# Kernel tuning notes

Measured on AMD Instinct MI355X. Metric: run time of the kernel, lower is better.

## Reference

```python
import jax, jax.numpy as jnp
import numpy as np

T_SCALE = 160
NUM_SAMPLE = 32
FEAT_DIM = 2048
HIDDEN = 512
N_CLASS = 20
BATCH = 8


def build_sample_mask(tscale=T_SCALE, ns=NUM_SAMPLE):
    # Vectorized version of _get_interp1d_mask (prop_boundary_ratio=0, num_sample_perbin=1).
    # Returns mask of shape [tscale, ns, start, end] (already transposed as in the torch code).
    s = np.arange(tscale)[:, None, None]           # start
    e = np.arange(tscale)[None, :, None]           # end
    k = np.arange(ns)[None, None, :]
    pos = s + (e - s) * k / (ns - 1.0)             # [T, T, ns] sample positions
    Sg, Eg, Kg = np.broadcast_arrays(s, e, k)
    posf = pos.ravel(); Sf = Sg.ravel(); Ef = Eg.ravel(); Kf = Kg.ravel()
    valid = Ef >= Sf
    frac, dn = np.modf(posf)
    dn = dn.astype(np.int64)
    up = np.ceil(posf).astype(np.int64)
    mask = np.zeros((tscale, ns, tscale, tscale), dtype=np.float32)
    m1 = valid & (dn >= 0) & (dn <= tscale - 1)
    np.add.at(mask, (dn[m1], Kf[m1], Sf[m1], Ef[m1]), (1.0 - frac[m1]).astype(np.float32))
    m2 = valid & (up >= 0) & (up <= tscale - 1)
    np.add.at(mask, (up[m2], Kf[m2], Sf[m2], Ef[m2]), frac[m2].astype(np.float32))
    return jnp.asarray(mask)


def conv1d(x, w, padding):
    # x: [B, Cin, T], w: [Cout, Cin, K]
    return jax.lax.conv_general_dilated(
        x, w, window_strides=(1,), padding=[(padding, padding)],
        dimension_numbers=("NCH", "OIH", "NCH"))


def setup_inputs() -> dict:
    key = jax.random.key(0)
    ks = jax.random.split(key, 6)
    x = jax.random.normal(ks[0], (BATCH, T_SCALE, FEAT_DIM), dtype=jnp.float32)
    w1 = jax.random.normal(ks[1], (HIDDEN, FEAT_DIM, 3), dtype=jnp.float32) * 0.02
    b1 = jnp.zeros((HIDDEN,), dtype=jnp.float32)
    wc = jax.random.normal(ks[2], (N_CLASS, HIDDEN, 1), dtype=jnp.float32) * 0.05
    wa = jax.random.normal(ks[3], (1, HIDDEN, 3), dtype=jnp.float32) * 0.05
    ba = jnp.zeros((1,), dtype=jnp.float32)
    sample_mask = build_sample_mask()  # [T, ns, T, T]
    return {"x": x, "sample_mask": sample_mask, "w1": w1, "b1": b1,
            "wc": wc, "wa": wa, "ba": ba}


def reference(x, sample_mask, w1, b1, wc, wa, ba):
    ns = NUM_SAMPLE
    q = ns // 4  # 8
    xp = jnp.transpose(x, (0, 2, 1))                   # [B, F, T]
    feat = jax.nn.relu(conv1d(xp, w1, 1) + b1[None, :, None])   # [B, H, T] (dropout = eval/identity)
    y_class = conv1d(feat, wc, 0)                      # [B, C, T]
    y_atn = conv1d(feat, wa, 1) + ba[None, :, None]    # [B, 1, T]
    # boundary matching: matmul against sparse interpolation mask
    out = jnp.einsum("bct,tkij->bckij", y_class, sample_mask)   # [B, C, ns, T, T]
    out_start = out[:, :, :q].mean(axis=2)
    out_mid = out[:, :, q:ns - q].mean(axis=2)
    out_end = out[:, :, ns - q:].mean(axis=2)
    bmn_class = jnp.concatenate((out_start, out_mid, out_end), axis=1)  # [B, 3C, T, T]
    sig = jax.nn.sigmoid(y_atn)
    x_fg = (sig * feat).sum(-1, keepdims=True) / (sig.sum(-1, keepdims=True) + 1e-8)  # [B, H, 1]
    y_fg = jnp.einsum("oh,bht->bot", wc[:, :, 0], x_fg)  # conv_class 1x1, no bias
    return (y_class, y_fg, bmn_class)
```

## Files before the change

### kernel.cpp

```cpp
#include <hip/hip_runtime.h>
#include <math.h>

#define TS 160
#define FEATD 2048
#define HID 512
#define NC 20
#define NB 8

typedef __attribute__((ext_vector_type(8))) short bfrag;
typedef __attribute__((ext_vector_type(4))) float f32x4;

static __device__ __forceinline__ unsigned short f2bf(float f) {
  unsigned int u = __float_as_uint(f);
  unsigned int r = (u + 0x7FFFu + ((u >> 16) & 1u)) >> 16;
  return (unsigned short)r;
}

static __device__ __forceinline__ void gload16(const void* g, void* l) {
  __builtin_amdgcn_global_load_lds((const __attribute__((address_space(1))) void*)g,
                                   (__attribute__((address_space(3))) void*)l, 16, 0, 0);
}

__global__ __launch_bounds__(256) void k_cvt(const float* __restrict__ x,
                                             const float* __restrict__ w1,
                                             unsigned short* __restrict__ xb,
                                             unsigned short* __restrict__ wb) {
  __shared__ float Ls[FEATD * 3];
  const int tid = threadIdx.x;
  if (blockIdx.x < 1296) {
    const int idx = blockIdx.x * 256 + tid;
    const int c = (idx & 255) * 8;
    const int row = idx >> 8;
    const int b = row / 162, pr = row - b * 162;
    unsigned short* o = xb + (size_t)row * FEATD + c;
    if (pr == 0 || pr == 161) {
      *(uint4*)o = make_uint4(0u, 0u, 0u, 0u);
    } else {
      const float* src = x + ((size_t)(b * TS + pr - 1)) * FEATD + c;
      float4 v0 = *(const float4*)src;
      float4 v1 = *(const float4*)(src + 4);
      unsigned short r[8] = {f2bf(v0.x), f2bf(v0.y), f2bf(v0.z), f2bf(v0.w),
                             f2bf(v1.x), f2bf(v1.y), f2bf(v1.z), f2bf(v1.w)};
      *(uint4*)o = *(const uint4*)r;
    }
  } else {
    const int h = blockIdx.x - 1296;
    const float4* src = (const float4*)(w1 + (size_t)h * (FEATD * 3));
    for (int e = tid; e < FEATD * 3 / 4; e += 256) ((float4*)Ls)[e] = src[e];
    __syncthreads();
    for (int oc = tid; oc < 768; oc += 256) {
      const int tap = oc >> 8;
      const int f0 = (oc & 255) * 8;
      unsigned short r[8];
      #pragma unroll
      for (int i = 0; i < 8; ++i) r[i] = f2bf(Ls[(f0 + i) * 3 + tap]);
      *(uint4*)&wb[((size_t)tap * HID + h) * FEATD + f0] = *(const uint4*)r;
    }
  }
}

__global__ __launch_bounds__(256) void k_wbuild(unsigned short* __restrict__ WT) {
  const int idx = blockIdx.x * 256 + threadIdx.x;
  const int tau = idx % 160;
  const int dd = (idx / 160) % 320;
  const int g = idx / (160 * 320);
  float w = 0.f;
  if (dd >= 160) {
    const int d = dd - 160;
    const int k0 = (g == 0) ? 0 : (g == 1 ? 8 : 24);
    const int k1 = (g == 0) ? 8 : (g == 1 ? 24 : 32);
    for (int k = k0; k < k1; ++k) {
      float p = (float)(d * k) / 31.0f;
      float a = fabsf(p - (float)tau);
      w += fmaxf(0.f, 1.f - a);
    }
    w *= (g == 1) ? 0.0625f : 0.125f;
  }
  WT[idx] = f2bf(w);
}

__global__ __launch_bounds__(256, 3) void k_conv_mfma(const unsigned short* __restrict__ xb,
                                                      const unsigned short* __restrict__ wb,
                                                      float* __restrict__ part) {
  const int bb = blockIdx.x;
  const int h0 = blockIdx.y * 64;
  const int kz = blockIdx.z;
  const int tid = threadIdx.x;
  const int wid = tid >> 6, lane = tid & 63;

  __shared__ unsigned short Alds[162 * 64];
  __shared__ unsigned short Blds[3 * 64 * 64];

  const unsigned short* xbb = xb + (size_t)bb * 162 * FEATD;
  const unsigned short* wbb = wb + (size_t)h0 * FEATD;

  f32x4 acc[5][2] = {};
  const int wr = wid >> 1, wc = wid & 1;

  for (int s = 0; s < 4; ++s) {
    const int f0 = kz * 256 + s * 64;
    #pragma unroll
    for (int is = 0; is < 5; ++is) {
      const int ci = is * 256 + wid * 64 + lane;
      const int row = ci >> 3, c = ci & 7;
      gload16(xbb + (size_t)row * FEATD + f0 + ((c ^ (row & 7)) << 3),
              (char*)Alds + (size_t)(is * 256 + wid * 64) * 16);
    }
    #pragma unroll
    for (int is = 0; is < 6; ++is) {
      const int ci = is * 256 + wid * 64 + lane;
      const int tap = ci >> 9, rr = (ci >> 3) & 63, c = ci & 7;
      gload16(wbb + (size_t)tap * (HID * FEATD) + (size_t)rr * FEATD + f0 + ((c ^ (rr & 7)) << 3),
              (char*)Blds + (size_t)(is * 256 + wid * 64) * 16);
    }
    if (tid < 16) {
      const int row = 160 + (tid >> 3), c = tid & 7;
      uint4 v = *(const uint4*)(xbb + (size_t)row * FEATD + f0 + ((c ^ (row & 7)) << 3));
      *(uint4*)((char*)Alds + row * 128 + c * 16) = v;
    }
    __syncthreads();

    #pragma unroll
    for (int tap = 0; tap < 3; ++tap) {
      #pragma unroll
      for (int kk = 0; kk < 2; ++kk) {
        const int cread = kk * 4 + (lane >> 4);
        bfrag bf0, bf1;
        {
          const int hh0 = wc * 32 + (lane & 15);
          const int hh1 = hh0 + 16;
          bf0 = *(const bfrag*)((char*)Blds + tap * 8192 + hh0 * 128 + ((cread ^ (hh0 & 7)) << 4));
          bf1 = *(const bfrag*)((char*)Blds + tap * 8192 + hh1 * 128 + ((cread ^ (hh1 & 7)) << 4));
        }
        #pragma unroll
        for (int mi = 0; mi < 5; ++mi) {
          const int rr = wr * 80 + mi * 16 + (lane & 15) + tap;
          bfrag af = *(const bfrag*)((char*)Alds + rr * 128 + ((cread ^ (rr & 7)) << 4));
          acc[mi][0] = __builtin_amdgcn_mfma_f32_16x16x32_bf16(af, bf0, acc[mi][0], 0, 0, 0);
          acc[mi][1] = __builtin_amdgcn_mfma_f32_16x16x32_bf16(af, bf1, acc[mi][1], 0, 0, 0);
        }
      }
    }
    __syncthreads();
  }

  float* pout = part + (size_t)kz * (NB * TS) * HID;
  #pragma unroll
  for (int mi = 0; mi < 5; ++mi) {
    const int r0 = bb * TS + wr * 80 + mi * 16 + (lane >> 4) * 4;
    #pragma unroll
    for (int ni = 0; ni < 2; ++ni) {
      const int c0 = h0 + wc * 32 + ni * 16 + (lane & 15);
      #pragma unroll
      for (int i = 0; i < 4; ++i)
        pout[(size_t)(r0 + i) * HID + c0] = acc[mi][ni][i];
    }
  }
}

__global__ __launch_bounds__(256) void k_bias_relu(const float* __restrict__ part,
                                                   const float* __restrict__ bias,
                                                   float* __restrict__ feat) {
  const int idx = blockIdx.x * 256 + threadIdx.x;
  const float4* p = (const float4*)part;
  float4 a = p[idx];
  #pragma unroll
  for (int k = 1; k < 8; ++k) {
    float4 v = p[(size_t)k * 163840 + idx];
    a.x += v.x; a.y += v.y; a.z += v.z; a.w += v.w;
  }
  const float4 bb = ((const float4*)bias)[idx & 127];
  float4 o;
  o.x = fmaxf(a.x + bb.x, 0.f);
  o.y = fmaxf(a.y + bb.y, 0.f);
  o.z = fmaxf(a.z + bb.z, 0.f);
  o.w = fmaxf(a.w + bb.w, 0.f);
  ((float4*)feat)[idx] = o;
}

__global__ __launch_bounds__(256) void k_head(const float* __restrict__ feat,
                                              const float* __restrict__ wc,
                                              const float* __restrict__ wa,
                                              const float* __restrict__ ba,
                                              float* __restrict__ y_class,
                                              float* __restrict__ y_atn) {
  __shared__ float wcs[NC * HID];
  __shared__ float was[HID * 3];
  const int tid = threadIdx.x;
  for (int e = tid; e < NC * HID; e += 256) wcs[e] = wc[e];
  for (int e = tid; e < HID * 3; e += 256) was[e] = wa[e];
  __syncthreads();
  const int wave = blockIdx.x * 4 + (tid >> 6);
  const int lane = tid & 63;
  const int b = wave / TS, t = wave - b * TS;
  const float* frow = &feat[((size_t)b * TS + t) * HID];
  float fc[8], fm[8], fp[8];
  #pragma unroll
  for (int i2 = 0; i2 < 8; ++i2) {
    int h = lane + 64 * i2;
    fc[i2] = frow[h];
    fm[i2] = (t > 0)      ? frow[h - HID] : 0.f;
    fp[i2] = (t < TS - 1) ? frow[h + HID] : 0.f;
  }
  #pragma unroll 4
  for (int c = 0; c < NC; ++c) {
    float p = 0.f;
    #pragma unroll
    for (int i2 = 0; i2 < 8; ++i2) p += fc[i2] * wcs[c * HID + lane + 64 * i2];
    #pragma unroll
    for (int off = 32; off; off >>= 1) p += __shfl_xor(p, off);
    if (lane == 0) y_class[((size_t)b * NC + c) * TS + t] = p;
  }
  float p = 0.f;
  #pragma unroll
  for (int i2 = 0; i2 < 8; ++i2) {
    int h = lane + 64 * i2;
    p += fm[i2] * was[h * 3 + 0] + fc[i2] * was[h * 3 + 1] + fp[i2] * was[h * 3 + 2];
  }
  #pragma unroll
  for (int off = 32; off; off >>= 1) p += __shfl_xor(p, off);
  if (lane == 0) y_atn[b * TS + t] = p + ba[0];
}

__global__ __launch_bounds__(256) void k_fg(const float* __restrict__ feat,
                                            const float* __restrict__ y_atn,
                                            const float* __restrict__ wc,
                                            float* __restrict__ y_fg) {
  const int b = blockIdx.x;
  const int tid = threadIdx.x;
  __shared__ float sig[TS];
  __shared__ float red[4];
  __shared__ float xfg[HID];
  float s = 0.f;
  if (tid < TS) { s = 1.f / (1.f + expf(-y_atn[b * TS + tid])); sig[tid] = s; }
  float r = s;
  #pragma unroll
  for (int off = 32; off; off >>= 1) r += __shfl_xor(r, off);
  if ((tid & 63) == 0) red[tid >> 6] = r;
  __syncthreads();
  const float inv = 1.f / (red[0] + red[1] + red[2] + red[3] + 1e-8f);
  for (int h = tid; h < HID; h += 256) {
    float a = 0.f;
    for (int t = 0; t < TS; ++t) a += sig[t] * feat[((size_t)b * TS + t) * HID + h];
    xfg[h] = a * inv;
  }
  __syncthreads();
  const int wv = tid >> 6, lane = tid & 63;
  for (int c = wv; c < NC; c += 4) {
    float p = 0.f;
    #pragma unroll
    for (int i2 = 0; i2 < 8; ++i2) {
      int h = lane + 64 * i2;
      p += wc[c * HID + h] * xfg[h];
    }
    #pragma unroll
    for (int off = 32; off; off >>= 1) p += __shfl_xor(p, off);
    if (lane == 0) y_fg[b * NC + c] = p;
  }
}

__global__ __launch_bounds__(256) void k_ysbuild(const float* __restrict__ y_class,
                                                 unsigned short* __restrict__ Ys) {
  const int idx = blockIdx.x * 256 + threadIdx.x;
  const int c8 = idx % 42;
  const int bc = (idx / 42) % 160;
  const int s = idx / (42 * 160);
  unsigned short r[8];
  #pragma unroll
  for (int e = 0; e < 8; ++e) {
    const int tpos = c8 * 8 + e + s;
    r[e] = (c8 * 8 + e < 336 && tpos < 160) ? f2bf(y_class[bc * 160 + tpos]) : (unsigned short)0;
  }
  *(uint4*)&Ys[((size_t)s * 160 + bc) * 336 + c8 * 8] = *(const uint4*)r;
}

__global__ __launch_bounds__(256, 1) void k_bmn_mfma(const unsigned short* __restrict__ Ys,
                                                     const unsigned short* __restrict__ WT,
                                                     float* __restrict__ bmn) {
  const int i = blockIdx.x;
  const int g = blockIdx.y;
  const int tid = threadIdx.x;
  const int wid = tid >> 6, lane = tid & 63;

  __shared__ char Alds[65536];
  __shared__ char Wlds[65536];

  const int s = i & 7;
  const char* ysb = (const char*)(Ys + (size_t)s * 160 * 336) + (size_t)(i - s) * 2;
  const char* wtb = (const char*)(WT + (size_t)g * 320 * 160) + (size_t)(160 - i) * 320;

  #pragma unroll
  for (int it = 0; it < 16; ++it) {
    const int idx = it * 256 + tid;
    int row = idx / 25, c = idx - row * 25;
    if (row > 159) row = 159;
    if (c > 19) c = 0;
    gload16(ysb + (size_t)row * 672 + c * 16, Alds + (size_t)idx * 16);
    gload16(wtb + (size_t)row * 320 + c * 16, Wlds + (size_t)idx * 16);
  }
  __syncthreads();

  const int wr = wid >> 1, wc = wid & 1;
  f32x4 acc[5][5] = {};

  #pragma unroll
  for (int ks = 0; ks < 5; ++ks) {
    const int cc = ks * 4 + (lane >> 4);
    bfrag bfr[5];
    #pragma unroll
    for (int nf = 0; nf < 5; ++nf) {
      const int j = wc * 80 + nf * 16 + (lane & 15);
      bfr[nf] = *(const bfrag*)(Wlds + (size_t)j * 400 + cc * 16);
    }
    #pragma unroll
    for (int mf = 0; mf < 5; ++mf) {
      const int r = wr * 80 + mf * 16 + (lane & 15);
      bfrag af = *(const bfrag*)(Alds + (size_t)r * 400 + cc * 16);
      #pragma unroll
      for (int nf = 0; nf < 5; ++nf)
        acc[mf][nf] = __builtin_amdgcn_mfma_f32_16x16x32_bf16(af, bfr[nf], acc[mf][nf], 0, 0, 0);
    }
  }

  #pragma unroll
  for (int mf = 0; mf < 5; ++mf) {
    const int r0 = wr * 80 + mf * 16 + (lane >> 4) * 4;
    #pragma unroll
    for (int reg = 0; reg < 4; ++reg) {
      const int r = r0 + reg;
      const int b = r / 20, c = r - b * 20;
      float* base = bmn + (((size_t)(b * 60 + g * 20 + c) * TS) + i) * TS;
      #pragma unroll
      for (int nf = 0; nf < 5; ++nf) {
        const int j = wc * 80 + nf * 16 + (lane & 15);
        base[j] = acc[mf][nf][reg];
      }
    }
  }
}

extern "C" void kernel_launch(void* const* d_in, const int* in_sizes, int n_in,
                              void* d_out, int out_size, void* d_ws, size_t ws_size,
                              hipStream_t stream) {
  const float* x  = (const float*)d_in[0];
  const float* w1 = (const float*)d_in[2];
  const float* b1 = (const float*)d_in[3];
  const float* wc = (const float*)d_in[4];
  const float* wa = (const float*)d_in[5];
  const float* ba = (const float*)d_in[6];

  float* out     = (float*)d_out;
  float* y_class = out;
  float* y_fg    = out + NB * NC * TS;
  float* bmn     = out + NB * NC * TS + NB * NC;

  float* part  = (float*)d_ws;
  float* feat  = part + 8 * NB * TS * HID;
  float* y_atn = feat + NB * TS * HID;
  unsigned short* xb = (unsigned short*)(y_atn + 2048);
  unsigned short* wb = xb + (size_t)NB * 162 * FEATD;
  unsigned short* WT = wb + (size_t)3 * HID * FEATD;
  unsigned short* Ys = WT + (size_t)3 * 320 * 160;

  k_wbuild<<<600, 256, 0, stream>>>(WT);
  k_cvt<<<1296 + 512, 256, 0, stream>>>(x, w1, xb, wb);
  k_conv_mfma<<<dim3(8, 8, 8), 256, 0, stream>>>(xb, wb, part);
  k_bias_relu<<<640, 256, 0, stream>>>(part, b1, feat);
  k_head<<<320, 256, 0, stream>>>(feat, wc, wa, ba, y_class, y_atn);
  k_fg<<<8, 256, 0, stream>>>(feat, y_atn, wc, y_fg);
  k_ysbuild<<<210, 256, 0, stream>>>(y_class, Ys);
  k_bmn_mfma<<<dim3(160, 3), 256, 0, stream>>>(Ys, WT, bmn);
}
```

Baseline: 80.73 us.

## Fuse prep kernels, store split-K partials as bf16, merge fg/ysbuild into bmn

Merges the WT weight-build kernel into the input conversion kernel. Conv split-K partial sums are now written as bf16 instead of fp32, which halves the partial-sum traffic read back in the bias-relu reduction. Folds the y_fg reduction and the shifted-Ys construction into a single tail kernel, so the bmn blocks build their A tiles directly from y_class. This removes three launches and one intermediate buffer, at the cost of rounding the partial sums to bf16 before they are summed (lower precision) and extra per-block conversion work in the tail.

After: 76.08 us. 5.8% less time.

```diff
diff --git a/kernel.cpp b/kernel.cpp
--- a/kernel.cpp
+++ b/kernel.cpp
@@ -15,20 +15,25 @@
   unsigned int r = (u + 0x7FFFu + ((u >> 16) & 1u)) >> 16;
   return (unsigned short)r;
 }
+static __device__ __forceinline__ float bf2f(unsigned short s) {
+  return __uint_as_float(((unsigned int)s) << 16);
+}
 
 static __device__ __forceinline__ void gload16(const void* g, void* l) {
   __builtin_amdgcn_global_load_lds((const __attribute__((address_space(1))) void*)g,
                                    (__attribute__((address_space(3))) void*)l, 16, 0, 0);
 }
 
-__global__ __launch_bounds__(256) void k_cvt(const float* __restrict__ x,
-                                             const float* __restrict__ w1,
-                                             unsigned short* __restrict__ xb,
-                                             unsigned short* __restrict__ wb) {
+__global__ __launch_bounds__(256) void k_prep(const float* __restrict__ x,
+                                              const float* __restrict__ w1,
+                                              unsigned short* __restrict__ xb,
+                                              unsigned short* __restrict__ wb,
+                                              unsigned short* __restrict__ WT) {
   __shared__ float Ls[FEATD * 3];
   const int tid = threadIdx.x;
-  if (blockIdx.x < 1296) {
-    const int idx = blockIdx.x * 256 + tid;
+  const int bx = blockIdx.x;
+  if (bx < 1296) {
+    const int idx = bx * 256 + tid;
     const int c = (idx & 255) * 8;
     const int row = idx >> 8;
     const int b = row / 162, pr = row - b * 162;
@@ -43,8 +48,8 @@
                              f2bf(v1.x), f2bf(v1.y), f2bf(v1.z), f2bf(v1.w)};
       *(uint4*)o = *(const uint4*)r;
     }
-  } else {
-    const int h = blockIdx.x - 1296;
+  } else if (bx < 1808) {
+    const int h = bx - 1296;
     const float4* src = (const float4*)(w1 + (size_t)h * (FEATD * 3));
     for (int e = tid; e < FEATD * 3 / 4; e += 256) ((float4*)Ls)[e] = src[e];
     __syncthreads();
@@ -56,32 +61,30 @@
       for (int i = 0; i < 8; ++i) r[i] = f2bf(Ls[(f0 + i) * 3 + tap]);
       *(uint4*)&wb[((size_t)tap * HID + h) * FEATD + f0] = *(const uint4*)r;
     }
-  }
-}
-
-__global__ __launch_bounds__(256) void k_wbuild(unsigned short* __restrict__ WT) {
-  const int idx = blockIdx.x * 256 + threadIdx.x;
-  const int tau = idx % 160;
-  const int dd = (idx / 160) % 320;
-  const int g = idx / (160 * 320);
-  float w = 0.f;
-  if (dd >= 160) {
-    const int d = dd - 160;
-    const int k0 = (g == 0) ? 0 : (g == 1 ? 8 : 24);
-    const int k1 = (g == 0) ? 8 : (g == 1 ? 24 : 32);
-    for (int k = k0; k < k1; ++k) {
-      float p = (float)(d * k) / 31.0f;
-      float a = fabsf(p - (float)tau);
-      w += fmaxf(0.f, 1.f - a);
-    }
-    w *= (g == 1) ? 0.0625f : 0.125f;
-  }
-  WT[idx] = f2bf(w);
+  } else {
+    const int idx = (bx - 1808) * 256 + tid;
+    const int tau = idx % 160;
+    const int dd = (idx / 160) % 320;
+    const int g = idx / (160 * 320);
+    float w = 0.f;
+    if (dd >= 160) {
+      const int d = dd - 160;
+      const int k0 = (g == 0) ? 0 : (g == 1 ? 8 : 24);
+      const int k1 = (g == 0) ? 8 : (g == 1 ? 24 : 32);
+      for (int k = k0; k < k1; ++k) {
+        float p = (float)(d * k) / 31.0f;
+        float a = fabsf(p - (float)tau);
+        w += fmaxf(0.f, 1.f - a);
+      }
+      w *= (g == 1) ? 0.0625f : 0.125f;
+    }
+    WT[idx] = f2bf(w);
+  }
 }
 
 __global__ __launch_bounds__(256, 3) void k_conv_mfma(const unsigned short* __restrict__ xb,
                                                       const unsigned short* __restrict__ wb,
-                                                      float* __restrict__ part) {
+                                                      unsigned short* __restrict__ part) {
   const int bb = blockIdx.x;
   const int h0 = blockIdx.y * 64;
   const int kz = blockIdx.z;
@@ -144,7 +147,7 @@
     __syncthreads();
   }
 
-  float* pout = part + (size_t)kz * (NB * TS) * HID;
+  unsigned short* pout = part + (size_t)kz * (NB * TS) * HID;
   #pragma unroll
   for (int mi = 0; mi < 5; ++mi) {
     const int r0 = bb * TS + wr * 80 + mi * 16 + (lane >> 4) * 4;
@@ -153,29 +156,35 @@
       const int c0 = h0 + wc * 32 + ni * 16 + (lane & 15);
       #pragma unroll
       for (int i = 0; i < 4; ++i)
-        pout[(size_t)(r0 + i) * HID + c0] = acc[mi][ni][i];
-    }
-  }
-}
-
-__global__ __launch_bounds__(256) void k_bias_relu(const float* __restrict__ part,
+        pout[(size_t)(r0 + i) * HID + c0] = f2bf(acc[mi][ni][i]);
+    }
+  }
+}
+
+__global__ __launch_bounds__(256) void k_bias_relu(const unsigned short* __restrict__ part,
                                                    const float* __restrict__ bias,
                                                    float* __restrict__ feat) {
   const int idx = blockIdx.x * 256 + threadIdx.x;
-  const float4* p = (const float4*)part;
-  float4 a = p[idx];
-  #pragma unroll
-  for (int k = 1; k < 8; ++k) {
-    float4 v = p[(size_t)k * 163840 + idx];
-    a.x += v.x; a.y += v.y; a.z += v.z; a.w += v.w;
-  }
-  const float4 bb = ((const float4*)bias)[idx & 127];
-  float4 o;
-  o.x = fmaxf(a.x + bb.x, 0.f);
-  o.y = fmaxf(a.y + bb.y, 0.f);
-  o.z = fmaxf(a.z + bb.z, 0.f);
-  o.w = fmaxf(a.w + bb.w, 0.f);
-  ((float4*)feat)[idx] = o;
+  const int h0 = (idx & 63) * 8;
+  float a[8];
+  {
+    float4 b0 = *(const float4*)&bias[h0];
+    float4 b1 = *(const float4*)&bias[h0 + 4];
+    a[0] = b0.x; a[1] = b0.y; a[2] = b0.z; a[3] = b0.w;
+    a[4] = b1.x; a[5] = b1.y; a[6] = b1.z; a[7] = b1.w;
+  }
+  #pragma unroll
+  for (int kz = 0; kz < 8; ++kz) {
+    uint4 v = *(const uint4*)&part[(size_t)kz * (NB * TS * HID) + (size_t)idx * 8];
+    const unsigned short* s = (const unsigned short*)&v;
+    #pragma unroll
+    for (int k = 0; k < 8; ++k) a[k] += bf2f(s[k]);
+  }
+  float4 o0, o1;
+  o0.x = fmaxf(a[0], 0.f); o0.y = fmaxf(a[1], 0.f); o0.z = fmaxf(a[2], 0.f); o0.w = fmaxf(a[3], 0.f);
+  o1.x = fmaxf(a[4], 0.f); o1.y = fmaxf(a[5], 0.f); o1.z = fmaxf(a[6], 0.f); o1.w = fmaxf(a[7], 0.f);
+  *(float4*)&feat[(size_t)idx * 8] = o0;
+  *(float4*)&feat[(size_t)idx * 8 + 4] = o1;
 }
 
 __global__ __launch_bounds__(256) void k_head(const float* __restrict__ feat,
@@ -222,85 +231,84 @@
   if (lane == 0) y_atn[b * TS + t] = p + ba[0];
 }
 
-__global__ __launch_bounds__(256) void k_fg(const float* __restrict__ feat,
-                                            const float* __restrict__ y_atn,
-                                            const float* __restrict__ wc,
-                                            float* __restrict__ y_fg) {
-  const int b = blockIdx.x;
+__global__ __launch_bounds__(256) void k_tail(const float* __restrict__ y_class,
+                                              const unsigned short* __restrict__ WT,
+                                              const float* __restrict__ feat,
+                                              const float* __restrict__ y_atn,
+                                              const float* __restrict__ wc,
+                                              float* __restrict__ y_fg,
+                                              float* __restrict__ bmn) {
+  __shared__ char Tlds[64000 + 65536];
   const int tid = threadIdx.x;
-  __shared__ float sig[TS];
-  __shared__ float red[4];
-  __shared__ float xfg[HID];
-  float s = 0.f;
-  if (tid < TS) { s = 1.f / (1.f + expf(-y_atn[b * TS + tid])); sig[tid] = s; }
-  float r = s;
-  #pragma unroll
-  for (int off = 32; off; off >>= 1) r += __shfl_xor(r, off);
-  if ((tid & 63) == 0) red[tid >> 6] = r;
-  __syncthreads();
-  const float inv = 1.f / (red[0] + red[1] + red[2] + red[3] + 1e-8f);
-  for (int h = tid; h < HID; h += 256) {
-    float a = 0.f;
-    for (int t = 0; t < TS; ++t) a += sig[t] * feat[((size_t)b * TS + t) * HID + h];
-    xfg[h] = a * inv;
-  }
-  __syncthreads();
-  const int wv = tid >> 6, lane = tid & 63;
-  for (int c = wv; c < NC; c += 4) {
-    float p = 0.f;
-    #pragma unroll
-    for (int i2 = 0; i2 < 8; ++i2) {
-      int h = lane + 64 * i2;
-      p += wc[c * HID + h] * xfg[h];
-    }
-    #pragma unroll
-    for (int off = 32; off; off >>= 1) p += __shfl_xor(p, off);
-    if (lane == 0) y_fg[b * NC + c] = p;
-  }
-}
-
-__global__ __launch_bounds__(256) void k_ysbuild(const float* __restrict__ y_class,
-                                                 unsigned short* __restrict__ Ys) {
-  const int idx = blockIdx.x * 256 + threadIdx.x;
-  const int c8 = idx % 42;
-  const int bc = (idx / 42) % 160;
-  const int s = idx / (42 * 160);
-  unsigned short r[8];
-  #pragma unroll
-  for (int e = 0; e < 8; ++e) {
-    const int tpos = c8 * 8 + e + s;
-    r[e] = (c8 * 8 + e < 336 && tpos < 160) ? f2bf(y_class[bc * 160 + tpos]) : (unsigned short)0;
-  }
-  *(uint4*)&Ys[((size_t)s * 160 + bc) * 336 + c8 * 8] = *(const uint4*)r;
-}
-
-__global__ __launch_bounds__(256, 1) void k_bmn_mfma(const unsigned short* __restrict__ Ys,
-                                                     const unsigned short* __restrict__ WT,
-                                                     float* __restrict__ bmn) {
+
+  if (blockIdx.y == 3) {
+    if (blockIdx.x >= 8) return;
+    const int b = blockIdx.x;
+    float* sig = (float*)Tlds;
+    float* red = sig + TS;
+    float* xfg = red + 8;
+    float s = 0.f;
+    if (tid < TS) { s = 1.f / (1.f + expf(-y_atn[b * TS + tid])); sig[tid] = s; }
+    float r = s;
+    #pragma unroll
+    for (int off = 32; off; off >>= 1) r += __shfl_xor(r, off);
+    if ((tid & 63) == 0) red[tid >> 6] = r;
+    __syncthreads();
+    const float inv = 1.f / (red[0] + red[1] + red[2] + red[3] + 1e-8f);
+    for (int h = tid; h < HID; h += 256) {
+      float a = 0.f;
+      for (int t = 0; t < TS; ++t) a += sig[t] * feat[((size_t)b * TS + t) * HID + h];
+      xfg[h] = a * inv;
+    }
+    __syncthreads();
+    const int wv = tid >> 6, lane = tid & 63;
+    for (int c = wv; c < NC; c += 4) {
+      float p = 0.f;
+      #pragma unroll
+      for (int i2 = 0; i2 < 8; ++i2) {
+        int h = lane + 64 * i2;
+        p += wc[c * HID + h] * xfg[h];
+      }
+      #pragma unroll
+      for (int off = 32; off; off >>= 1) p += __shfl_xor(p, off);
+      if (lane == 0) y_fg[b * NC + c] = p;
+    }
+    return;
+  }
+
+  char* Alds = Tlds;
+  char* Wlds = Tlds + 64000;
   const int i = blockIdx.x;
   const int g = blockIdx.y;
-  const int tid = threadIdx.x;
   const int wid = tid >> 6, lane = tid & 63;
 
-  __shared__ char Alds[65536];
-  __shared__ char Wlds[65536];
-
-  const int s = i & 7;
-  const char* ysb = (const char*)(Ys + (size_t)s * 160 * 336) + (size_t)(i - s) * 2;
-  const char* wtb = (const char*)(WT + (size_t)g * 320 * 160) + (size_t)(160 - i) * 320;
-
+  const char* wtb = (const char*)WT + (size_t)g * 102400 + (size_t)(160 - i) * 320;
   #pragma unroll
   for (int it = 0; it < 16; ++it) {
     const int idx = it * 256 + tid;
     int row = idx / 25, c = idx - row * 25;
     if (row > 159) row = 159;
     if (c > 19) c = 0;
-    gload16(ysb + (size_t)row * 672 + c * 16, Alds + (size_t)idx * 16);
     gload16(wtb + (size_t)row * 320 + c * 16, Wlds + (size_t)idx * 16);
   }
+  for (int e = 0; e < 13; ++e) {
+    const int ci = e * 256 + tid;
+    if (ci < 3200) {
+      const int row = ci / 20, c = ci - row * 20;
+      const int tb = i + c * 8;
+      const float* yr = y_class + (size_t)row * TS;
+      unsigned short r8[8];
+      #pragma unroll
+      for (int k = 0; k < 8; ++k) {
+        const int t = tb + k;
+        r8[k] = (t < TS) ? f2bf(yr[t]) : (unsigned short)0;
+      }
+      *(uint4*)(Alds + (size_t)row * 400 + c * 16) = *(const uint4*)r8;
+    }
+  }
   __syncthreads();
 
-  const int wr = wid >> 1, wc = wid & 1;
+  const int wr = wid >> 1, wcq = wid & 1;
   f32x4 acc[5][5] = {};
 
   #pragma unroll
@@ -309,7 +317,7 @@
     bfrag bfr[5];
     #pragma unroll
     for (int nf = 0; nf < 5; ++nf) {
-      const int j = wc * 80 + nf * 16 + (lane & 15);
+      const int j = wcq * 80 + nf * 16 + (lane & 15);
       bfr[nf] = *(const bfrag*)(Wlds + (size_t)j * 400 + cc * 16);
     }
     #pragma unroll
@@ -332,7 +340,7 @@
       float* base = bmn + (((size_t)(b * 60 + g * 20 + c) * TS) + i) * TS;
       #pragma unroll
       for (int nf = 0; nf < 5; ++nf) {
-        const int j = wc * 80 + nf * 16 + (lane & 15);
+        const int j = wcq * 80 + nf * 16 + (lane & 15);
         base[j] = acc[mf][nf][reg];
       }
     }
@@ -354,20 +362,16 @@
   float* y_fg    = out + NB * NC * TS;
   float* bmn     = out + NB * NC * TS + NB * NC;
 
-  float* part  = (float*)d_ws;
-  float* feat  = part + 8 * NB * TS * HID;
+  unsigned short* part = (unsigned short*)d_ws;
+  float* feat  = (float*)((char*)d_ws + (size_t)8 * NB * TS * HID * 2);
   float* y_atn = feat + NB * TS * HID;
   unsigned short* xb = (unsigned short*)(y_atn + 2048);
   unsigned short* wb = xb + (size_t)NB * 162 * FEATD;
   unsigned short* WT = wb + (size_t)3 * HID * FEATD;
-  unsigned short* Ys = WT + (size_t)3 * 320 * 160;
-
-  k_wbuild<<<600, 256, 0, stream>>>(WT);
-  k_cvt<<<1296 + 512, 256, 0, stream>>>(x, w1, xb, wb);
+
+  k_prep<<<1808 + 600, 256, 0, stream>>>(x, w1, xb, wb, WT);
   k_conv_mfma<<<dim3(8, 8, 8), 256, 0, stream>>>(xb, wb, part);
-  k_bias_relu<<<640, 256, 0, stream>>>(part, b1, feat);
+  k_bias_relu<<<320, 256, 0, stream>>>(part, b1, feat);
   k_head<<<320, 256, 0, stream>>>(feat, wc, wa, ba, y_class, y_atn);
-  k_fg<<<8, 256, 0, stream>>>(feat, y_atn, wc, y_fg);
-  k_ysbuild<<<210, 256, 0, stream>>>(y_class, Ys);
-  k_bmn_mfma<<<dim3(160, 3), 256, 0, stream>>>(Ys, WT, bmn);
-}
+  k_tail<<<dim3(160, 4), 256, 0, stream>>>(y_class, WT, feat, y_atn, wc, y_fg, bmn);
+}
```
